# Kernel tuning notes

Hardware: AMD Instinct MI355X
Metric: run time of the kernel (lower is better)

Reference implementation:

```python
import jax, jax.numpy as jnp
import numpy as np

B, D_IN, D_HID, D_OUT, N_EXP, K = 32768, 256, 512, 256, 16, 2


def setup_inputs() -> dict:
    key = jax.random.key(0)
    ks = jax.random.split(key, 5)
    s_in = 1.0 / np.sqrt(D_IN)
    s_hid = 1.0 / np.sqrt(D_HID)
    return {
        "x": jax.random.normal(ks[0], (B, D_IN), jnp.float32),
        "Wg": jax.random.normal(ks[1], (D_IN, N_EXP), jnp.float32) * s_in,
        "bg": jnp.zeros((N_EXP,), jnp.float32),
        "W1": jax.random.normal(ks[2], (N_EXP, D_IN, D_HID), jnp.float32) * s_in,
        "b1": jnp.zeros((N_EXP, D_HID), jnp.float32),
        "W2": jax.random.normal(ks[3], (N_EXP, D_HID, D_OUT), jnp.float32) * s_hid,
        "b2": jnp.zeros((N_EXP, D_OUT), jnp.float32),
    }


def reference(x, Wg, bg, W1, b1, W2, b2):
    # Gating: linear -> softmax -> top-k -> renormalize (inference path, no noise)
    logits = x @ Wg + bg                       # [B, E]
    probs = jax.nn.softmax(logits, axis=-1)
    top_w, top_idx = jax.lax.top_k(probs, K)   # [B, K]
    top_w = top_w / jnp.sum(top_w, axis=-1, keepdims=True)

    # Expert MLPs (evaluate all experts densely, then gather selected outputs;
    # same math as masked gather -> MLP -> weighted scatter-add)
    h = jax.nn.relu(jnp.einsum('bi,eih->beh', x, W1) + b1[None])  # [B, E, H]
    y_all = jnp.einsum('beh,eho->beo', h, W2) + b2[None]          # [B, E, O]

    y_sel = jnp.take_along_axis(y_all, top_idx[:, :, None], axis=1)  # [B, K, O]
    return jnp.sum(y_sel * top_w[:, :, None], axis=1)                # [B, O]
```

## Files before the change

### kernel.cpp

```cpp
#include <hip/hip_runtime.h>
#include <stdint.h>

#define BTOK 32768
#define DIN 256
#define DHID 512
#define DOUT 256
#define NEXP 16
#define BM 64
#define CH 32
#define NCH 16
#define SLOTS 168

typedef __attribute__((ext_vector_type(8))) short bf16x8;
typedef __attribute__((ext_vector_type(4))) float f32x4;

__device__ __forceinline__ unsigned short f2bf(float f){
  unsigned u = __builtin_bit_cast(unsigned, f);
  u = u + 0x7FFFu + ((u >> 16) & 1u);
  return (unsigned short)(u >> 16);
}
__device__ __forceinline__ float bf2f(unsigned short h){
  return __builtin_bit_cast(float, (unsigned)h << 16);
}
__device__ __forceinline__ void gload16(const void* g, void* l){
  __builtin_amdgcn_global_load_lds((const __attribute__((address_space(1))) unsigned int*)g,
                                   (__attribute__((address_space(3))) unsigned int*)l, 16, 0, 0);
}

__global__ __launch_bounds__(256) void transpose_cvt(const float* __restrict__ src,
                                                     unsigned short* __restrict__ dst,
                                                     int R, int C){
  __shared__ float t[32][33];
  int e = blockIdx.z, r0 = blockIdx.y * 32, c0 = blockIdx.x * 32;
  int lx = threadIdx.x & 31, ly = threadIdx.x >> 5;
  const float* s = src + (size_t)e * R * C;
  unsigned short* d = dst + (size_t)e * R * C;
#pragma unroll
  for (int i = 0; i < 4; i++){ int r = ly + i * 8; t[r][lx] = s[(size_t)(r0 + r) * C + c0 + lx]; }
  __syncthreads();
#pragma unroll
  for (int i = 0; i < 4; i++){ int r = ly + i * 8; d[(size_t)(c0 + r) * R + r0 + lx] = f2bf(t[lx][r]); }
}

__global__ __launch_bounds__(256) void transpose_cvt_w2(const float* __restrict__ src,
                                                        unsigned short* __restrict__ dst){
  __shared__ float t[32][33];
  int e = blockIdx.z, r0 = blockIdx.y * 32, c0 = blockIdx.x * 32;
  int lx = threadIdx.x & 31, ly = threadIdx.x >> 5;
  const float* s = src + (size_t)e * DHID * DOUT;
  unsigned short* d = dst + (size_t)e * DHID * DOUT + (r0 >> 5) * (DOUT * CH);
#pragma unroll
  for (int i = 0; i < 4; i++){ int r = ly + i * 8; t[r][lx] = s[(size_t)(r0 + r) * DOUT + c0 + lx]; }
  __syncthreads();
#pragma unroll
  for (int i = 0; i < 4; i++){ int rr = ly + i * 8; d[(size_t)(c0 + rr) * CH + lx] = f2bf(t[lx][rr]); }
}

__global__ __launch_bounds__(256) void gating_kernel(const float* __restrict__ x,
                                                     const float* __restrict__ Wg,
                                                     const float* __restrict__ bg,
                                                     unsigned short* __restrict__ x_bf,
                                                     int* __restrict__ top_idx,
                                                     float* __restrict__ top_w,
                                                     int* __restrict__ counts){
  __shared__ float WgT[16][256];
  __shared__ int hist[16];
  int tid = threadIdx.x;
#pragma unroll
  for (int j = 0; j < 4; j++){
    float4 wv = *(const float4*)(Wg + tid * 16 + j * 4);
    WgT[j * 4 + 0][tid] = wv.x; WgT[j * 4 + 1][tid] = wv.y;
    WgT[j * 4 + 2][tid] = wv.z; WgT[j * 4 + 3][tid] = wv.w;
  }
  if (tid < 16) hist[tid] = 0;
  __syncthreads();
  int wid = tid >> 6, lane = tid & 63;

  for (int t = 0; t < 16; t++){
    int tok = blockIdx.x * 64 + wid * 16 + t;
    const float4 xv = *(const float4*)(x + (size_t)tok * DIN + lane * 4);
    ushort4 xb; xb.x = f2bf(xv.x); xb.y = f2bf(xv.y); xb.z = f2bf(xv.z); xb.w = f2bf(xv.w);
    *(ushort4*)(x_bf + (size_t)tok * DIN + lane * 4) = xb;
    float logit[16];
#pragma unroll
    for (int e = 0; e < 16; e++){
      const float4 wv = *(const float4*)(&WgT[e][lane * 4]);
      float v = xv.x * wv.x + xv.y * wv.y + xv.z * wv.z + xv.w * wv.w;
#pragma unroll
      for (int off = 32; off; off >>= 1) v += __shfl_xor(v, off, 64);
      logit[e] = v + bg[e];
    }
    if (lane == 0){
      int i1 = 0; float v1 = logit[0];
#pragma unroll
      for (int e = 1; e < 16; e++) if (logit[e] > v1){ v1 = logit[e]; i1 = e; }
      int i2 = -1; float v2 = -3.4e38f;
#pragma unroll
      for (int e = 0; e < 16; e++) if (e != i1 && logit[e] > v2){ v2 = logit[e]; i2 = e; }
      float tt = expf(v2 - v1);
      float w1 = 1.0f / (1.0f + tt);
      float w2 = tt / (1.0f + tt);
      top_idx[tok * 2] = i1; top_idx[tok * 2 + 1] = i2;
      top_w[tok * 2] = w1;  top_w[tok * 2 + 1] = w2;
      atomicAdd(&hist[i1], 1); atomicAdd(&hist[i2], 1);
    }
  }
  __syncthreads();
  if (tid < 16) atomicAdd(&counts[tid], hist[tid]);
}

__global__ void prefix_kernel(const int* __restrict__ counts, int* __restrict__ offsets,
                              int* __restrict__ cursor, int* __restrict__ bm_e,
                              int* __restrict__ bm_start, int* __restrict__ bm_end){
  int lane = threadIdx.x & 63;
  int c = (lane < 16) ? counts[lane] : 0;
  int s = c;
#pragma unroll
  for (int off = 1; off < 16; off <<= 1){ int o = __shfl_up(s, off, 64); if (lane >= off) s += o; }
  int start = s - c;
  if (lane < 16){ offsets[lane] = start; cursor[lane] = start; }
  int nb = (c + BM - 1) >> 6;
  int nb_partner = __shfl(nb, lane ^ 8, 64);
  if (lane < 8){
    int filled = nb + nb_partner;
    if (filled > SLOTS) filled = SLOTS;
    for (int i = filled; i < SLOTS; i++) bm_e[lane * SLOTS + i] = -1;
  }
  if (lane < 16){
    int sbase = (lane < 8) ? 0 : nb_partner;
    int xcd = lane & 7;
    for (int b = 0; b < nb; b++){
      int idx = xcd * SLOTS + sbase + b;
      if (sbase + b < SLOTS){
        bm_e[idx] = lane; bm_start[idx] = start + b * BM; bm_end[idx] = start + c;
      }
    }
  }
}

__global__ __launch_bounds__(256) void scatter_kernel(const int* __restrict__ top_idx,
                                                      const float* __restrict__ top_w,
                                                      int* __restrict__ cursor,
                                                      int* __restrict__ pair_tok,
                                                      float* __restrict__ pair_w){
  __shared__ int hist[16], base[16], rank[16];
  int tid = threadIdx.x;
  if (tid < 16){ hist[tid] = 0; rank[tid] = 0; }
  __syncthreads();
  int t = blockIdx.x * 256 + tid;
  int e0 = top_idx[t * 2], e1 = top_idx[t * 2 + 1];
  float w0 = top_w[t * 2], w1 = top_w[t * 2 + 1];
  atomicAdd(&hist[e0], 1); atomicAdd(&hist[e1], 1);
  __syncthreads();
  if (tid < 16) base[tid] = atomicAdd(&cursor[tid], hist[tid]);
  __syncthreads();
  int r0 = atomicAdd(&rank[e0], 1);
  int p0 = base[e0] + r0;
  pair_tok[p0] = t; pair_w[p0] = w0;
  int r1 = atomicAdd(&rank[e1], 1);
  int p1 = base[e1] + r1;
  pair_tok[p1] = t | (1 << 16); pair_w[p1] = w1;
}

__global__ __launch_bounds__(512, 4) void moe_gemm_kernel(
    const unsigned short* __restrict__ x_bf,
    const unsigned short* __restrict__ W1t,
    const unsigned short* __restrict__ W2c,
    const float* __restrict__ b1,
    const float* __restrict__ b2,
    const int* __restrict__ pair_tok, const float* __restrict__ pair_w,
    const int* __restrict__ bm_e, const int* __restrict__ bm_start,
    const int* __restrict__ bm_end,
    unsigned short* __restrict__ ypair){
  int xcd = blockIdx.x & 7, slot = blockIdx.x >> 3;
  int bmi = xcd * SLOTS + slot;
  int e = bm_e[bmi];
  if (e < 0) return;
  int rs = bm_start[bmi], re = bm_end[bmi];

  __shared__ unsigned short w1s[2][CH * 256];
  __shared__ unsigned short w2s[2][256 * CH];
  __shared__ unsigned short hs[BM * CH];

  int tid = threadIdx.x, wid = tid >> 6, lane = tid & 63, lr = lane & 15, lh = lane >> 4;
  int mg = wid >> 1, ng = wid & 1;
  char* hsb = (char*)hs;
  const char* gW1 = (const char*)(W1t + (size_t)e * DHID * DIN);
  const char* gW2 = (const char*)(W2c + (size_t)e * DOUT * DHID);

  int o1 = ((tid >> 5) * 512) + (((tid & 31) ^ ((tid >> 5) & 7)) * 16);
  int o2;
  { int p = tid >> 3, q = (tid & 7) ^ (p & 7);
    o2 = (p * 2 + (q >> 2)) * 64 + (q & 3) * 16; }

#define STAGE(c, sl) {                                                    \
    const char* s1 = gW1 + (size_t)(c) * 16384;                           \
    const char* s2 = gW2 + (size_t)(c) * 16384;                           \
    char* d1 = (char*)w1s[sl]; char* d2 = (char*)w2s[sl];                 \
    gload16(s1 + o1,        d1 + tid * 16);                               \
    gload16(s1 + o1 + 8192, d1 + tid * 16 + 8192);                        \
    gload16(s2 + o2,        d2 + tid * 16);                               \
    gload16(s2 + o2 + 8192, d2 + tid * 16 + 8192);                        \
  }

  bf16x8 xr[8];
  {
    int g0 = rs + 16 * mg + lr;
    int gc = g0 < re ? g0 : (re - 1);
    int tok = pair_tok[gc] & 0xFFFF;
    const unsigned short* xrow = x_bf + (size_t)tok * DIN + lh * 8;
#pragma unroll
    for (int ks = 0; ks < 8; ks++) xr[ks] = *(const bf16x8*)(xrow + ks * 32);
  }

  f32x4 acc[8];
#pragma unroll
  for (int i = 0; i < 8; i++) acc[i] = (f32x4){0.f, 0.f, 0.f, 0.f};

  STAGE(0, 0);
  __syncthreads();

  for (int c = 0; c < NCH; c++){
    int sl = c & 1;
    if (c + 1 < NCH) STAGE(c + 1, sl ^ 1);

    {
      const char* w1b = (const char*)w1s[sl];
      f32x4 hacc = (f32x4){0.f, 0.f, 0.f, 0.f};
      int hrow = 16 * ng + lr;
#pragma unroll
      for (int ks = 0; ks < 8; ks++){
        bf16x8 b = *(const bf16x8*)(w1b + ((hrow * 512 + ks * 64 + lh * 16) ^ ((hrow & 7) << 4)));
        hacc = __builtin_amdgcn_mfma_f32_16x16x32_bf16(xr[ks], b, hacc, 0, 0, 0);
      }
      float b1v = b1[e * DHID + c * CH + 16 * ng + lr];
      int col2 = (16 * ng + lr) * 2;
#pragma unroll
      for (int r = 0; r < 4; r++){
        int mm = 16 * mg + lh * 4 + r;
        float v = fmaxf(hacc[r] + b1v, 0.f);
        int adr = (mm >> 1) * 128 + ((((mm & 1) << 6) + col2) ^ (((mm >> 1) & 7) << 4));
        *(unsigned short*)(hsb + adr) = f2bf(v);
      }
    }
    __syncthreads();

    {
      int mm = 16 * mg + lr;
      int hadr = (mm >> 1) * 128 + ((((mm & 1) << 6) + (lh << 4)) ^ (((mm >> 1) & 7) << 4));
      bf16x8 ha = *(const bf16x8*)(hsb + hadr);
      const char* w2b = (const char*)w2s[sl];
#pragma unroll
      for (int nt = 0; nt < 8; nt++){
        int n = 128 * ng + nt * 16 + lr;
        int adr = (n >> 1) * 128 + ((((n & 1) << 6) + (lh << 4)) ^ (((n >> 1) & 7) << 4));
        bf16x8 b = *(const bf16x8*)(w2b + adr);
        acc[nt] = __builtin_amdgcn_mfma_f32_16x16x32_bf16(ha, b, acc[nt], 0, 0, 0);
      }
    }
    __syncthreads();
  }

  {
    float wrow[4]; int yrow[4]; int valid[4];
#pragma unroll
    for (int r = 0; r < 4; r++){
      int gg = rs + 16 * mg + lh * 4 + r;
      valid[r] = gg < re;
      int gc = valid[r] ? gg : (re - 1);
      int pt = pair_tok[gc];
      yrow[r] = (pt & 0xFFFF) * 2 + (pt >> 16);
      wrow[r] = valid[r] ? pair_w[gc] : 0.f;
    }
#pragma unroll
    for (int nt = 0; nt < 8; nt++){
      int col = 128 * ng + nt * 16 + lr;
      float b2v = b2[e * DOUT + col];
#pragma unroll
      for (int r = 0; r < 4; r++){
        if (valid[r])
          ypair[(size_t)yrow[r] * DOUT + col] = f2bf(wrow[r] * (acc[nt][r] + b2v));
      }
    }
  }
#undef STAGE
}

__global__ __launch_bounds__(256) void combine_kernel(const unsigned short* __restrict__ yp,
                                                      float* __restrict__ out){
  int idx = blockIdx.x * 256 + threadIdx.x;
  int t = idx >> 6;
  int c4 = (idx & 63) << 2;
  ushort4 a = *(const ushort4*)(yp + (size_t)(t * 2) * DOUT + c4);
  ushort4 b = *(const ushort4*)(yp + (size_t)(t * 2 + 1) * DOUT + c4);
  float4 o;
  o.x = bf2f(a.x) + bf2f(b.x);
  o.y = bf2f(a.y) + bf2f(b.y);
  o.z = bf2f(a.z) + bf2f(b.z);
  o.w = bf2f(a.w) + bf2f(b.w);
  *(float4*)(out + (size_t)t * DOUT + c4) = o;
}

extern "C" void kernel_launch(void* const* d_in, const int* in_sizes, int n_in,
                              void* d_out, int out_size, void* d_ws, size_t ws_size,
                              hipStream_t stream){
  (void)in_sizes; (void)n_in; (void)out_size; (void)ws_size;
  const float* x  = (const float*)d_in[0];
  const float* Wg = (const float*)d_in[1];
  const float* bg = (const float*)d_in[2];
  const float* W1 = (const float*)d_in[3];
  const float* b1 = (const float*)d_in[4];
  const float* W2 = (const float*)d_in[5];
  const float* b2 = (const float*)d_in[6];
  float* out = (float*)d_out;
  char* ws = (char*)d_ws;

  unsigned short* x_bf  = (unsigned short*)(ws);
  unsigned short* W1t   = (unsigned short*)(ws + 16777216);
  unsigned short* W2ck  = (unsigned short*)(ws + 20971520);
  unsigned short* ypair = (unsigned short*)(ws + 25165824);
  int*   top_idx  = (int*)  (ws + 58720256);
  float* top_w    = (float*)(ws + 58982400);
  int*   pair_tok = (int*)  (ws + 59244544);
  float* pair_w   = (float*)(ws + 59506688);
  int*   counts   = (int*)  (ws + 60030976);
  int*   offsets  = (int*)  (ws + 60031040);
  int*   cursor   = (int*)  (ws + 60031104);
  int*   bm_e     = (int*)  (ws + 60031232);
  int*   bm_start = (int*)  (ws + 60036608);
  int*   bm_end   = (int*)  (ws + 60041984);

  hipMemsetAsync(counts, 0, 64, stream);
  transpose_cvt<<<dim3(16, 8, 16), 256, 0, stream>>>(W1, W1t, 256, 512);
  transpose_cvt_w2<<<dim3(8, 16, 16), 256, 0, stream>>>(W2, W2ck);
  gating_kernel<<<512, 256, 0, stream>>>(x, Wg, bg, x_bf, top_idx, top_w, counts);
  prefix_kernel<<<1, 64, 0, stream>>>(counts, offsets, cursor, bm_e, bm_start, bm_end);
  scatter_kernel<<<128, 256, 0, stream>>>(top_idx, top_w, cursor, pair_tok, pair_w);
  moe_gemm_kernel<<<8 * SLOTS, 512, 0, stream>>>(x_bf, W1t, W2ck, b1, b2, pair_tok, pair_w,
                                                 bm_e, bm_start, bm_end, ypair);
  combine_kernel<<<8192, 256, 0, stream>>>(ypair, out);
}
```

Baseline: 166.9 us.

## Enlarge MoE GEMM tiles to 128 rows with 32x32 MFMA and wider chunks

Doubles the token block to 128 rows and the hidden chunk to 64, switching the expert MLP from 16x16x32 to 32x32x16 bf16 MFMA with matching swizzled LDS layouts and W2 pre-layout. Weight chunks per expert are loaded half as many times per token, which raises arithmetic intensity and halves the barrier count. Syncthreads are replaced with explicit waitcnt plus s_barrier. In exchange, LDS use and register pressure go up, occupancy drops to one block per SIMD group, and fewer, larger blocks waste more padding on partial tiles.

```diff
diff --git a/kernel.cpp b/kernel.cpp
--- a/kernel.cpp
+++ b/kernel.cpp
@@ -6,13 +6,13 @@
 #define DHID 512
 #define DOUT 256
 #define NEXP 16
-#define BM 64
-#define CH 32
-#define NCH 16
-#define SLOTS 168
+#define BM 128
+#define CH 64
+#define NCH 8
+#define SLOTS 96
 
 typedef __attribute__((ext_vector_type(8))) short bf16x8;
-typedef __attribute__((ext_vector_type(4))) float f32x4;
+typedef __attribute__((ext_vector_type(16))) float f32x16;
 
 __device__ __forceinline__ unsigned short f2bf(float f){
   unsigned u = __builtin_bit_cast(unsigned, f);
@@ -48,7 +48,7 @@
   int e = blockIdx.z, r0 = blockIdx.y * 32, c0 = blockIdx.x * 32;
   int lx = threadIdx.x & 31, ly = threadIdx.x >> 5;
   const float* s = src + (size_t)e * DHID * DOUT;
-  unsigned short* d = dst + (size_t)e * DHID * DOUT + (r0 >> 5) * (DOUT * CH);
+  unsigned short* d = dst + (size_t)e * DHID * DOUT + (r0 >> 6) * (DOUT * CH) + (r0 & 32);
 #pragma unroll
   for (int i = 0; i < 4; i++){ int r = ly + i * 8; t[r][lx] = s[(size_t)(r0 + r) * DOUT + c0 + lx]; }
   __syncthreads();
@@ -119,7 +119,7 @@
   for (int off = 1; off < 16; off <<= 1){ int o = __shfl_up(s, off, 64); if (lane >= off) s += o; }
   int start = s - c;
   if (lane < 16){ offsets[lane] = start; cursor[lane] = start; }
-  int nb = (c + BM - 1) >> 6;
+  int nb = (c + BM - 1) >> 7;
   int nb_partner = __shfl(nb, lane ^ 8, 64);
   if (lane < 8){
     int filled = nb + nb_partner;
@@ -162,7 +162,7 @@
   pair_tok[p1] = t | (1 << 16); pair_w[p1] = w1;
 }
 
-__global__ __launch_bounds__(512, 4) void moe_gemm_kernel(
+__global__ __launch_bounds__(512, 1) void moe_gemm_kernel(
     const unsigned short* __restrict__ x_bf,
     const unsigned short* __restrict__ W1t,
     const unsigned short* __restrict__ W2c,
@@ -182,104 +182,124 @@
   __shared__ unsigned short w2s[2][256 * CH];
   __shared__ unsigned short hs[BM * CH];
 
-  int tid = threadIdx.x, wid = tid >> 6, lane = tid & 63, lr = lane & 15, lh = lane >> 4;
-  int mg = wid >> 1, ng = wid & 1;
+  int tid = threadIdx.x, wid = tid >> 6, lane = tid & 63;
+  int l31 = lane & 31, l5 = lane >> 5;
+  int mg = wid >> 1, hg = wid & 1;
   char* hsb = (char*)hs;
   const char* gW1 = (const char*)(W1t + (size_t)e * DHID * DIN);
   const char* gW2 = (const char*)(W2c + (size_t)e * DOUT * DHID);
 
-  int o1 = ((tid >> 5) * 512) + (((tid & 31) ^ ((tid >> 5) & 7)) * 16);
-  int o2;
-  { int p = tid >> 3, q = (tid & 7) ^ (p & 7);
-    o2 = (p * 2 + (q >> 2)) * 64 + (q & 3) * 16; }
+  int o1, o2;
+  { int r = tid >> 5; o1 = r * 512 + (((tid & 31) ^ (r & 15)) * 16); }
+  { int p = tid >> 4; int q = (tid & 15) ^ (p & 15);
+    o2 = (p * 2 + (q >> 3)) * 128 + (q & 7) * 16; }
 
 #define STAGE(c, sl) {                                                    \
-    const char* s1 = gW1 + (size_t)(c) * 16384;                           \
-    const char* s2 = gW2 + (size_t)(c) * 16384;                           \
+    const char* s1 = gW1 + (size_t)(c) * 32768;                           \
+    const char* s2 = gW2 + (size_t)(c) * 32768;                           \
     char* d1 = (char*)w1s[sl]; char* d2 = (char*)w2s[sl];                 \
-    gload16(s1 + o1,        d1 + tid * 16);                               \
-    gload16(s1 + o1 + 8192, d1 + tid * 16 + 8192);                        \
-    gload16(s2 + o2,        d2 + tid * 16);                               \
-    gload16(s2 + o2 + 8192, d2 + tid * 16 + 8192);                        \
-  }
-
-  bf16x8 xr[8];
+    _Pragma("unroll")                                                     \
+    for (int k = 0; k < 4; k++){                                          \
+      gload16(s1 + o1 + k * 8192, d1 + tid * 16 + k * 8192);              \
+      gload16(s2 + o2 + k * 8192, d2 + tid * 16 + k * 8192);              \
+    } }
+
+  bf16x8 xr[16];
   {
-    int g0 = rs + 16 * mg + lr;
+    int g0 = rs + mg * 32 + l31;
     int gc = g0 < re ? g0 : (re - 1);
     int tok = pair_tok[gc] & 0xFFFF;
-    const unsigned short* xrow = x_bf + (size_t)tok * DIN + lh * 8;
-#pragma unroll
-    for (int ks = 0; ks < 8; ks++) xr[ks] = *(const bf16x8*)(xrow + ks * 32);
-  }
-
-  f32x4 acc[8];
-#pragma unroll
-  for (int i = 0; i < 8; i++) acc[i] = (f32x4){0.f, 0.f, 0.f, 0.f};
+    const unsigned short* xrow = x_bf + (size_t)tok * DIN + l5 * 8;
+#pragma unroll
+    for (int ks = 0; ks < 16; ks++) xr[ks] = *(const bf16x8*)(xrow + ks * 16);
+  }
+
+  const f32x16 fzero = {0.f,0.f,0.f,0.f,0.f,0.f,0.f,0.f,0.f,0.f,0.f,0.f,0.f,0.f,0.f,0.f};
+  f32x16 acc[4];
+  acc[0] = fzero; acc[1] = fzero; acc[2] = fzero; acc[3] = fzero;
 
   STAGE(0, 0);
-  __syncthreads();
+  asm volatile("s_waitcnt vmcnt(0)" ::: "memory");
+  __builtin_amdgcn_sched_barrier(0);
+  __builtin_amdgcn_s_barrier();
+  __builtin_amdgcn_sched_barrier(0);
+
+  int hid = hg * 32 + l31;
+  int swzA = (hid & 15) << 4;
 
   for (int c = 0; c < NCH; c++){
     int sl = c & 1;
     if (c + 1 < NCH) STAGE(c + 1, sl ^ 1);
 
+    float b1v = b1[e * DHID + c * CH + hid];
+
     {
       const char* w1b = (const char*)w1s[sl];
-      f32x4 hacc = (f32x4){0.f, 0.f, 0.f, 0.f};
-      int hrow = 16 * ng + lr;
-#pragma unroll
-      for (int ks = 0; ks < 8; ks++){
-        bf16x8 b = *(const bf16x8*)(w1b + ((hrow * 512 + ks * 64 + lh * 16) ^ ((hrow & 7) << 4)));
-        hacc = __builtin_amdgcn_mfma_f32_16x16x32_bf16(xr[ks], b, hacc, 0, 0, 0);
-      }
-      float b1v = b1[e * DHID + c * CH + 16 * ng + lr];
-      int col2 = (16 * ng + lr) * 2;
-#pragma unroll
-      for (int r = 0; r < 4; r++){
-        int mm = 16 * mg + lh * 4 + r;
-        float v = fmaxf(hacc[r] + b1v, 0.f);
-        int adr = (mm >> 1) * 128 + ((((mm & 1) << 6) + col2) ^ (((mm >> 1) & 7) << 4));
+      f32x16 h0 = fzero, h1 = fzero;
+#pragma unroll
+      for (int ks = 0; ks < 16; ks += 2){
+        bf16x8 bA = *(const bf16x8*)(w1b + hid * 512 + ((ks * 32 + l5 * 16) ^ swzA));
+        bf16x8 bB = *(const bf16x8*)(w1b + hid * 512 + (((ks + 1) * 32 + l5 * 16) ^ swzA));
+        h0 = __builtin_amdgcn_mfma_f32_32x32x16_bf16(xr[ks], bA, h0, 0, 0, 0);
+        h1 = __builtin_amdgcn_mfma_f32_32x32x16_bf16(xr[ks + 1], bB, h1, 0, 0, 0);
+      }
+      f32x16 hsum = h0 + h1;
+      int h2 = hg * 64 + l31 * 2;
+#pragma unroll
+      for (int r = 0; r < 16; r++){
+        int tk = mg * 32 + (r & 3) + ((r >> 2) << 3) + (l5 << 2);
+        float v = fmaxf(hsum[r] + b1v, 0.f);
+        int adr = (tk >> 1) * 256 + ((((tk & 1) << 7) + h2) ^ (((tk >> 1) & 15) << 4));
         *(unsigned short*)(hsb + adr) = f2bf(v);
       }
     }
-    __syncthreads();
+    asm volatile("s_waitcnt lgkmcnt(0)" ::: "memory");
+    __builtin_amdgcn_sched_barrier(0);
+    __builtin_amdgcn_s_barrier();
+    __builtin_amdgcn_sched_barrier(0);
 
     {
-      int mm = 16 * mg + lr;
-      int hadr = (mm >> 1) * 128 + ((((mm & 1) << 6) + (lh << 4)) ^ (((mm >> 1) & 7) << 4));
-      bf16x8 ha = *(const bf16x8*)(hsb + hadr);
       const char* w2b = (const char*)w2s[sl];
-#pragma unroll
-      for (int nt = 0; nt < 8; nt++){
-        int n = 128 * ng + nt * 16 + lr;
-        int adr = (n >> 1) * 128 + ((((n & 1) << 6) + (lh << 4)) ^ (((n >> 1) & 7) << 4));
-        bf16x8 b = *(const bf16x8*)(w2b + adr);
-        acc[nt] = __builtin_amdgcn_mfma_f32_16x16x32_bf16(ha, b, acc[nt], 0, 0, 0);
-      }
-    }
-    __syncthreads();
+      int tk = mg * 32 + l31;
+      int hswz = ((tk >> 1) & 15) << 4;
+      int hbase = (tk >> 1) * 256;
+      int hhi = (tk & 1) << 7;
+#pragma unroll
+      for (int ks = 0; ks < 4; ks++){
+        bf16x8 ha = *(const bf16x8*)(hsb + hbase + ((hhi + ks * 32 + l5 * 16) ^ hswz));
+#pragma unroll
+        for (int ot = 0; ot < 4; ot++){
+          int n = hg * 128 + ot * 32 + l31;
+          int adr = (n >> 1) * 256 + ((((n & 1) << 7) + ks * 32 + l5 * 16) ^ (((n >> 1) & 15) << 4));
+          bf16x8 bb = *(const bf16x8*)(w2b + adr);
+          acc[ot] = __builtin_amdgcn_mfma_f32_32x32x16_bf16(ha, bb, acc[ot], 0, 0, 0);
+        }
+      }
+    }
+    if (c + 1 < NCH){
+      asm volatile("s_waitcnt vmcnt(0) lgkmcnt(0)" ::: "memory");
+      __builtin_amdgcn_sched_barrier(0);
+      __builtin_amdgcn_s_barrier();
+      __builtin_amdgcn_sched_barrier(0);
+    }
   }
 
   {
-    float wrow[4]; int yrow[4]; int valid[4];
-#pragma unroll
-    for (int r = 0; r < 4; r++){
-      int gg = rs + 16 * mg + lh * 4 + r;
-      valid[r] = gg < re;
-      int gc = valid[r] ? gg : (re - 1);
-      int pt = pair_tok[gc];
-      yrow[r] = (pt & 0xFFFF) * 2 + (pt >> 16);
-      wrow[r] = valid[r] ? pair_w[gc] : 0.f;
-    }
-#pragma unroll
-    for (int nt = 0; nt < 8; nt++){
-      int col = 128 * ng + nt * 16 + lr;
-      float b2v = b2[e * DOUT + col];
-#pragma unroll
-      for (int r = 0; r < 4; r++){
-        if (valid[r])
-          ypair[(size_t)yrow[r] * DOUT + col] = f2bf(wrow[r] * (acc[nt][r] + b2v));
+    float b2v[4];
+#pragma unroll
+    for (int ot = 0; ot < 4; ot++) b2v[ot] = b2[e * DOUT + hg * 128 + ot * 32 + l31];
+#pragma unroll
+    for (int r = 0; r < 16; r++){
+      int tl = mg * 32 + (r & 3) + ((r >> 2) << 3) + (l5 << 2);
+      int gg = rs + tl;
+      if (gg < re){
+        int pt = pair_tok[gg];
+        int yrow = (pt & 0xFFFF) * 2 + (pt >> 16);
+        float w = pair_w[gg];
+        unsigned short* yp = ypair + (size_t)yrow * DOUT + hg * 128 + l31;
+#pragma unroll
+        for (int ot = 0; ot < 4; ot++)
+          yp[ot * 32] = f2bf(w * (acc[ot][r] + b2v[ot]));
       }
     }
   }
```

After: 159.5 us. -4.4%, faster.
